# Kernel tuning notes

Hardware: AMD Instinct MI355X
Metric: run time of the kernel (lower is better)

## Reference

```python
import jax, jax.numpy as jnp
import numpy as np

B = 1024
FEAT_C = [64, 64, 128, 256, 512]    # channel dim of each intermediate feature map
SPATIAL = [1024, 1024, 256, 64, 16]  # flattened HxW of each map (32x32 input)
STRIDES = [1, 1, 2, 4, 8]
NUM_CLASS = 10


def _conv(x, w, b, s):
    y = jax.lax.conv_general_dilated(x, w, (s, s), 'SAME',
                                     dimension_numbers=('NCHW', 'OIHW', 'NCHW'))
    return y + b[None, :, None, None]


def setup_inputs() -> dict:
    key = jax.random.key(0)
    ks = iter(jax.random.split(key, 64))
    nrm = lambda shape, scale=1.0: jax.random.normal(next(ks), shape, jnp.float32) * scale
    inp = {'x': nrm((B, 3, 32, 32))}
    inp['noise_w'] = nrm((15, 3, 3, 3), 0.1)
    inp['noise_b'] = nrm((15,), 0.01)
    for i, (c, s) in enumerate(zip(FEAT_C, SPATIAL)):
        inp[f'feat_w{i}'] = nrm((c, 3, 3, 3), 0.2)
        inp[f'feat_b{i}'] = nrm((c,), 0.01)
        inp[f'mu_w{i}'] = nrm((NUM_CLASS, s), 1.0 / np.sqrt(s))
        inp[f'mu_b{i}'] = nrm((NUM_CLASS,), 0.01)
        inp[f'std_w{i}'] = nrm((NUM_CLASS, s), 1.0 / np.sqrt(s))
        inp[f'std_b{i}'] = nrm((NUM_CLASS,), 0.01)
    inp['clf_w'] = nrm((1, 5), 0.5)
    inp['clf_b'] = nrm((1,), 0.01)
    return inp


def _forward(x, noise_w, noise_b, feat_ws, feat_bs, mu_ws, mu_bs, std_ws, std_bs, clf_w, clf_b):
    Bsz = x.shape[0]
    # noised_img = x.repeat([1,5,1,1]) + noise_layer(x)   -> [B,15,32,32]
    noised = jnp.tile(x, (1, 5, 1, 1)) + _conv(x, noise_w, noise_b, 1)
    ekey = jax.random.key(42)
    scores, means, stds = [], [], []
    for i in range(5):
        xi = noised[:, 3 * i:3 * (i + 1)]
        # stand-in for pretrained_model.intermediate_forward -> [B, C_i, S_i]
        f = _conv(xi, feat_ws[i], feat_bs[i], STRIDES[i]).reshape(Bsz, FEAT_C[i], -1)
        # Linear over flattened-spatial dim then transpose(1,2): [B, 10, C_i]
        x_mean = jnp.einsum('bcs,ks->bkc', f, mu_ws[i]) + mu_bs[i][None, :, None]
        x_std = jnp.einsum('bcs,ks->bkc', f, std_ws[i]) + std_bs[i][None, :, None]
        # original builds dense diag(std)^2 [B,10,C,C]; diagonal exploited analytically
        var = x_std * x_std                       # diag entries of x_variance (== scale_tril)
        eps = jax.random.normal(jax.random.fold_in(ekey, i), x_mean.shape, x_mean.dtype)
        d = var * eps                             # sample - mean = scale_tril @ eps (diagonal)
        # -0.5 * d^T inv(diag(var)) d, inverse done analytically instead of torch.inverse
        mahal = -0.5 * jnp.sum(d * d / var, axis=-1)   # [B, 10]
        idx = jnp.argmax(mahal, axis=1)
        scores.append(jnp.max(mahal, axis=1))
        means.append(jnp.take_along_axis(x_mean, idx[:, None, None], axis=1)[:, 0, :])
        stds.append(jnp.take_along_axis(x_std, idx[:, None, None], axis=1)[:, 0, :])
    score_stack = jnp.stack(scores, axis=1)       # [B, 5]
    out = (score_stack @ clf_w.T + clf_b)[:, 0]   # classifier Linear(5,1), squeeze(-1)
    return out, means, stds


def reference(x, noise_w, noise_b,
              feat_w0, feat_b0, mu_w0, mu_b0, std_w0, std_b0,
              feat_w1, feat_b1, mu_w1, mu_b1, std_w1, std_b1,
              feat_w2, feat_b2, mu_w2, mu_b2, std_w2, std_b2,
              feat_w3, feat_b3, mu_w3, mu_b3, std_w3, std_b3,
              feat_w4, feat_b4, mu_w4, mu_b4, std_w4, std_b4,
              clf_w, clf_b):
    feat_ws = [feat_w0, feat_w1, feat_w2, feat_w3, feat_w4]
    feat_bs = [feat_b0, feat_b1, feat_b2, feat_b3, feat_b4]
    mu_ws = [mu_w0, mu_w1, mu_w2, mu_w3, mu_w4]
    mu_bs = [mu_b0, mu_b1, mu_b2, mu_b3, mu_b4]
    std_ws = [std_w0, std_w1, std_w2, std_w3, std_w4]
    std_bs = [std_b0, std_b1, std_b2, std_b3, std_b4]
    out, means, stds = _forward(x, noise_w, noise_b, feat_ws, feat_bs,
                                mu_ws, mu_bs, std_ws, std_bs, clf_w, clf_b)
    return (out, *means, *stds)
```

## Files before the change

kernel.cpp:

```cpp
#include <hip/hip_runtime.h>
#include <cstdint>

#define B_SZ 1024
#define NTHR 640

__host__ __device__ inline void tf2x32(uint32_t k0, uint32_t k1,
                                       uint32_t x0, uint32_t x1,
                                       uint32_t& o0, uint32_t& o1) {
  uint32_t ks2 = 0x1BD11BDAu ^ k0 ^ k1;
#define TF_RND(r) { x0 += x1; x1 = (x1 << (r)) | (x1 >> (32 - (r))); x1 ^= x0; }
  x0 += k0; x1 += k1;
  TF_RND(13) TF_RND(15) TF_RND(26) TF_RND(6)
  x0 += k1; x1 += ks2 + 1u;
  TF_RND(17) TF_RND(29) TF_RND(16) TF_RND(24)
  x0 += ks2; x1 += k0 + 2u;
  TF_RND(13) TF_RND(15) TF_RND(26) TF_RND(6)
  x0 += k0; x1 += k1 + 3u;
  TF_RND(17) TF_RND(29) TF_RND(16) TF_RND(24)
  x0 += k1; x1 += ks2 + 4u;
  TF_RND(13) TF_RND(15) TF_RND(26) TF_RND(6)
  x0 += ks2; x1 += k0 + 5u;
#undef TF_RND
  o0 = x0; o1 = x1;
}

__device__ inline float erfinv_f32(float x) {
  float w = -log1pf(-x * x);
  float p;
  if (w < 5.0f) {
    w -= 2.5f;
    p = 2.81022636e-08f;
    p = fmaf(p, w, 3.43273939e-07f);
    p = fmaf(p, w, -3.5233877e-06f);
    p = fmaf(p, w, -4.39150654e-06f);
    p = fmaf(p, w, 0.00021858087f);
    p = fmaf(p, w, -0.00125372503f);
    p = fmaf(p, w, -0.00417768164f);
    p = fmaf(p, w, 0.246640727f);
    p = fmaf(p, w, 1.50140941f);
  } else {
    w = sqrtf(w) - 3.0f;
    p = -0.000200214257f;
    p = fmaf(p, w, 0.000100950558f);
    p = fmaf(p, w, 0.00134934322f);
    p = fmaf(p, w, -0.00367342844f);
    p = fmaf(p, w, 0.00573950773f);
    p = fmaf(p, w, -0.0076224613f);
    p = fmaf(p, w, 0.00943887047f);
    p = fmaf(p, w, 1.00167406f);
    p = fmaf(p, w, 2.83297682f);
  }
  return p * x;
}

__device__ inline float jax_normal_pt(uint32_t k0, uint32_t k1, uint32_t e) {
  uint32_t o0, o1;
  tf2x32(k0, k1, 0u, e, o0, o1);
  uint32_t bits = o0 ^ o1;
  float f = __uint_as_float((bits >> 9) | 0x3f800000u) - 1.0f;
  const float LO = -0.99999994f;
  float u = fmaxf(LO, fmaf(f, 2.0f, LO));
  return 1.41421356f * erfinv_f32(u);
}

struct OodArgs {
  const float* x;
  const float* noise_w;
  const float* noise_b;
  const float* feat_w[5];
  const float* feat_b[5];
  const float* mu_w[5];
  const float* mu_b[5];
  const float* std_w[5];
  const float* std_b[5];
  float* mean_out[5];
  float* std_out[5];
  float* scores;
  float* gws;
  uint32_t fk0[5], fk1[5];
};

#define PITCH 35
#define CHSZ  (34 * PITCH)
#define XSZ   (3 * CHSZ)

#define A_XP   0
#define A_XI   3570
#define A_NW   7140
#define A_NB   7221
#define A_SMEM 7224

template<int S, int STRIDE>
__device__ __forceinline__ void stageA(const OodArgs& A_, float* smem, int i) {
  constexpr int Wd = 32 / STRIDE;

  const int b = blockIdx.x;
  const int t = threadIdx.x;

  float* s_xp = smem + A_XP;
  float* s_xi = smem + A_XI;
  float* s_nw = smem + A_NW;
  float* s_nb = smem + A_NB;

  for (int p = t; p < 2 * XSZ; p += NTHR) smem[p] = 0.0f;
  if (t < 81) s_nw[t] = A_.noise_w[81 * i + t];
  if (t < 3)  s_nb[t] = A_.noise_b[3 * i + t];
  __syncthreads();
  const float* xb = A_.x + (size_t)b * 3072;
  for (int p = t; p < 3072; p += NTHR) {
    int ci = p >> 10; int rr = p & 1023; int yy = rr >> 5; int xx = rr & 31;
    s_xp[ci * CHSZ + (yy + 1) * PITCH + (xx + 1)] = xb[p];
  }
  __syncthreads();

  #pragma unroll
  for (int co = 0; co < 3; ++co) {
    float nwr[27];
    #pragma unroll
    for (int j = 0; j < 27; ++j) nwr[j] = s_nw[co * 27 + j];
    const float nb = s_nb[co];
    for (int p = t; p < 1024; p += NTHR) {
      const int base = (p >> 5) * PITCH + (p & 31);
      float a = nb;
      #pragma unroll
      for (int c2 = 0; c2 < 3; ++c2) {
        #pragma unroll
        for (int q = 0; q < 9; ++q)
          a = fmaf(s_xp[c2 * CHSZ + base + (q / 3) * PITCH + (q % 3)],
                   nwr[c2 * 9 + q], a);
      }
      s_xi[co * CHSZ + base + PITCH + 1] = a + s_xp[co * CHSZ + base + PITCH + 1];
    }
  }
  __syncthreads();

  const int G  = t >> 5;
  const int ss = t & 31;
  const int wh = G & 1;
  const int kk = G >> 1;
  const float* wsrc = (wh ? A_.std_w[i] : A_.mu_w[i]) + kk * S;
  float* gdst = A_.gws + (size_t)(b * 5 + i) * 560;

  if constexpr (STRIDE == 1) {
    const float* wr = wsrc + ss * 32;
    const int rbase0 = ss * PITCH;
    #pragma unroll
    for (int ci = 0; ci < 3; ++ci) {
      const int rb = ci * CHSZ + rbase0;
      float acc[10];
      #pragma unroll
      for (int j = 0; j < 10; ++j) acc[j] = 0.0f;
      float Av[3], Bv[3], Cv[3];
      #pragma unroll
      for (int u = 0; u < 3; ++u) {
        Av[u] = s_xi[rb + u * PITCH + 0];
        Bv[u] = s_xi[rb + u * PITCH + 1];
      }

#define WCOMP(V, L) ((L) == 0 ? (V).x : (L) == 1 ? (V).y : (L) == 2 ? (V).z : (V).w)
#define STEP(X, P, Q, R, W0) { \
    _Pragma("unroll") \
    for (int u = 0; u < 3; ++u) R[u] = s_xi[rb + u * PITCH + (X) + 2]; \
    const float w0c = WCOMP(W0, (X) & 3); \
    _Pragma("unroll") \
    for (int dy = 0; dy < 3; ++dy) { \
      acc[dy*3+0] = fmaf(w0c, P[dy], acc[dy*3+0]); \
      acc[dy*3+1] = fmaf(w0c, Q[dy], acc[dy*3+1]); \
      acc[dy*3+2] = fmaf(w0c, R[dy], acc[dy*3+2]); \
    } \
    if (ci == 0) acc[9] += w0c; \
  }
#define G4_0(c) { const float4 w0 = *(const float4*)(wr + (c)); \
    STEP((c)+0, Av, Bv, Cv, w0) STEP((c)+1, Bv, Cv, Av, w0) \
    STEP((c)+2, Cv, Av, Bv, w0) STEP((c)+3, Av, Bv, Cv, w0) }
#define G4_1(c) { const float4 w0 = *(const float4*)(wr + (c)); \
    STEP((c)+0, Bv, Cv, Av, w0) STEP((c)+1, Cv, Av, Bv, w0) \
    STEP((c)+2, Av, Bv, Cv, w0) STEP((c)+3, Bv, Cv, Av, w0) }
#define G4_2(c) { const float4 w0 = *(const float4*)(wr + (c)); \
    STEP((c)+0, Cv, Av, Bv, w0) STEP((c)+1, Av, Bv, Cv, w0) \
    STEP((c)+2, Bv, Cv, Av, w0) STEP((c)+3, Cv, Av, Bv, w0) }

      G4_0(0) G4_1(4) G4_2(8) G4_0(12) G4_1(16) G4_2(20) G4_0(24) G4_1(28)

#undef G4_0
#undef G4_1
#undef G4_2
#undef STEP
#undef WCOMP
      #pragma unroll
      for (int j = 0; j < 10; ++j) {
        float v = acc[j];
        v += __shfl_xor(v,  1, 64);
        v += __shfl_xor(v,  2, 64);
        v += __shfl_xor(v,  4, 64);
        v += __shfl_xor(v,  8, 64);
        v += __shfl_xor(v, 16, 64);
        acc[j] = v;
      }
      if (ss == 0) {
        #pragma unroll
        for (int j = 0; j < 9; ++j)
          gdst[(wh * 10 + kk) * 27 + ci * 9 + j] = acc[j];
        if (ci == 0) gdst[540 + wh * 10 + kk] = acc[9];
      }
    }
  } else {
    constexpr int PER = (S >= 32) ? (S / 32) : 1;
    #pragma unroll
    for (int ci = 0; ci < 3; ++ci) {
      float acc[10];
      #pragma unroll
      for (int j = 0; j < 10; ++j) acc[j] = 0.0f;
      if (S >= 32 || ss < S) {
        #pragma unroll
        for (int u = 0; u < PER; ++u) {
          const int s  = (S >= 32) ? (ss * PER + u) : ss;
          const int yo = s / Wd, xo = s % Wd;
          const float wx = wsrc[s];
          #pragma unroll
          for (int dy = 0; dy < 3; ++dy) {
            const int base = ci * CHSZ + (yo * STRIDE + dy + 1) * PITCH + (xo * STRIDE + 1);
            #pragma unroll
            for (int dx = 0; dx < 3; ++dx)
              acc[dy * 3 + dx] = fmaf(wx, s_xi[base + dx], acc[dy * 3 + dx]);
          }
          if (ci == 0) acc[9] += wx;
        }
      }
      #pragma unroll
      for (int j = 0; j < 10; ++j) {
        float v = acc[j];
        v += __shfl_xor(v,  1, 64);
        v += __shfl_xor(v,  2, 64);
        v += __shfl_xor(v,  4, 64);
        v += __shfl_xor(v,  8, 64);
        v += __shfl_xor(v, 16, 64);
        acc[j] = v;
      }
      if (ss == 0) {
        #pragma unroll
        for (int j = 0; j < 9; ++j)
          gdst[(wh * 10 + kk) * 27 + ci * 9 + j] = acc[j];
        if (ci == 0) gdst[540 + wh * 10 + kk] = acc[9];
      }
    }
  }
}

__global__ __launch_bounds__(NTHR, 8)
void ood_a(OodArgs A_) {
  __shared__ float smem[A_SMEM];
  const int y = blockIdx.y;
  switch (y) {
    case 0:
    case 1: stageA<1024, 1>(A_, smem, y); break;
    case 2: stageA< 256, 2>(A_, smem, 2); break;
    case 3: stageA<  64, 4>(A_, smem, 3); break;
    default: stageA< 16, 8>(A_, smem, 4); break;
  }
}

template<int I, int C>
__device__ __forceinline__ void stageB(const OodArgs& A_, float* smem) {
  const int b = blockIdx.x;
  const int t = threadIdx.x;

  float* s_g   = smem;
  float* s_rs  = smem + 540;
  float* s_std = smem + 560;
  float* s_pt  = smem + 560 + 10 * C;
  int*   s_idx = (int*)(smem + 570 + 10 * C);

  const float* feat_w = A_.feat_w[I];
  const float* feat_b = A_.feat_b[I];
  const uint32_t fk0 = A_.fk0[I], fk1 = A_.fk1[I];

  const float* gsrc = A_.gws + (size_t)(b * 5 + I) * 560;
  for (int p = t; p < 560; p += 320) smem[p] = gsrc[p];
  __syncthreads();

  for (int v = t; v < 10 * C; v += 320) {
    const int k2 = v / C; const int c = v - k2 * C;
    const float* fw = feat_w + c * 27;
    float a2 = 0.0f;
    #pragma unroll
    for (int j = 0; j < 27; ++j) a2 = fmaf(s_g[(10 + k2) * 27 + j], fw[j], a2);
    a2 = fmaf(feat_b[c], s_rs[10 + k2], a2) + A_.std_b[I][k2];
    s_std[v] = a2;
  }
  __syncthreads();

  {
    const int g  = t >> 6;
    const int ln = t & 63;
    float m0 = 0.0f, m1 = 0.0f;
    for (int c = ln; c < C; c += 64) {
      {
        const float sd  = s_std[g * C + c];
        const float eps = jax_normal_pt(fk0, fk1, (uint32_t)((b * 10 + g) * C + c));
        m0 = fmaf(sd * sd, eps * eps, m0);
      }
      {
        const float sd  = s_std[(g + 5) * C + c];
        const float eps = jax_normal_pt(fk0, fk1, (uint32_t)((b * 10 + g + 5) * C + c));
        m1 = fmaf(sd * sd, eps * eps, m1);
      }
    }
    #pragma unroll
    for (int off = 32; off > 0; off >>= 1) {
      m0 += __shfl_down(m0, off, 64);
      m1 += __shfl_down(m1, off, 64);
    }
    if (ln == 0) { s_pt[g] = m0; s_pt[g + 5] = m1; }
  }
  __syncthreads();
  if (t == 0) {
    float best = -INFINITY; int bi = 0;
    #pragma unroll
    for (int k2 = 0; k2 < 10; ++k2) {
      float m = -0.5f * s_pt[k2];
      if (m > best) { best = m; bi = k2; }
    }
    A_.scores[b * 5 + I] = best;
    *s_idx = bi;
  }
  __syncthreads();

  const int idx = *s_idx;
  for (int c = t; c < C; c += 320) {
    const float* fw = feat_w + c * 27;
    float a1 = 0.0f;
    #pragma unroll
    for (int j = 0; j < 27; ++j) a1 = fmaf(s_g[idx * 27 + j], fw[j], a1);
    a1 = fmaf(feat_b[c], s_rs[idx], a1) + A_.mu_b[I][idx];
    A_.mean_out[I][(size_t)b * C + c] = a1;
    A_.std_out[I][(size_t)b * C + c]  = s_std[idx * C + c];
  }
}

__global__ __launch_bounds__(320)
void ood_b(OodArgs A_) {
  __shared__ float smem[571 + 5120];
  switch (blockIdx.y) {
    case 0: stageB<0,  64>(A_, smem); break;
    case 1: stageB<1,  64>(A_, smem); break;
    case 2: stageB<2, 128>(A_, smem); break;
    case 3: stageB<3, 256>(A_, smem); break;
    default: stageB<4, 512>(A_, smem); break;
  }
}

__global__ void ood_clf(const float* __restrict__ scores,
                        const float* __restrict__ clf_w,
                        const float* __restrict__ clf_b,
                        float* __restrict__ out) {
  int b = blockIdx.x * blockDim.x + threadIdx.x;
  if (b < B_SZ) {
    float acc = clf_b[0];
    #pragma unroll
    for (int i = 0; i < 5; ++i) acc = fmaf(scores[b * 5 + i], clf_w[i], acc);
    out[b] = acc;
  }
}

extern "C" void kernel_launch(void* const* d_in, const int* in_sizes, int n_in,
                              void* d_out, int out_size, void* d_ws, size_t ws_size,
                              hipStream_t stream) {
  (void)in_sizes; (void)n_in; (void)out_size; (void)ws_size;
  const float* clf_w = (const float*)d_in[33];
  const float* clf_b = (const float*)d_in[34];
  float* out = (float*)d_out;
  float* ws  = (float*)d_ws;

  OodArgs A_;
  A_.x       = (const float*)d_in[0];
  A_.noise_w = (const float*)d_in[1];
  A_.noise_b = (const float*)d_in[2];
  const size_t NMEAN = 1048576;
  const size_t moff[5] = {1024, 66560, 132096, 263168, 525312};
  for (int i = 0; i < 5; ++i) {
    A_.feat_w[i]   = (const float*)d_in[3 + 6 * i];
    A_.feat_b[i]   = (const float*)d_in[4 + 6 * i];
    A_.mu_w[i]     = (const float*)d_in[5 + 6 * i];
    A_.mu_b[i]     = (const float*)d_in[6 + 6 * i];
    A_.std_w[i]    = (const float*)d_in[7 + 6 * i];
    A_.std_b[i]    = (const float*)d_in[8 + 6 * i];
    A_.mean_out[i] = out + moff[i];
    A_.std_out[i]  = out + moff[i] + NMEAN;
    tf2x32(0u, 42u, 0u, (uint32_t)i, A_.fk0[i], A_.fk1[i]);
  }
  A_.scores = ws;
  A_.gws    = ws + 5120;

  ood_a<<<dim3(B_SZ, 5), NTHR, 0, stream>>>(A_);
  ood_b<<<dim3(B_SZ, 5), 320, 0, stream>>>(A_);
  ood_clf<<<(B_SZ + 255) / 256, 256, 0, stream>>>(A_.scores, clf_w, clf_b, out);
}
```

Measured before the change: 306.9 us.

## Fuse projection-collapse stage and scoring stage into one kernel via shared memory

Merges the two per-(batch, feature) kernels into a single kernel. The collapsed G and rowsum vectors stay in shared memory instead of going through a global workspace, and the std/eps/argmin stage reuses the freed image buffer region. This removes a kernel launch and the global round trip of the 560-float intermediate. The second stage now runs with 640 threads, so the eps loop handles one class per 64-lane group. The smem overlay of s_std onto the image buffers relies on the barrier placement, and the fused kernel's register and LDS needs may lower occupancy.

```diff
diff --git a/kernel.cpp b/kernel.cpp
--- a/kernel.cpp
+++ b/kernel.cpp
@@ -76,7 +76,6 @@
   float* mean_out[5];
   float* std_out[5];
   float* scores;
-  float* gws;
   uint32_t fk0[5], fk1[5];
 };
 
@@ -84,23 +83,29 @@
 #define CHSZ  (34 * PITCH)
 #define XSZ   (3 * CHSZ)
 
-#define A_XP   0
-#define A_XI   3570
-#define A_NW   7140
-#define A_NB   7221
-#define A_SMEM 7224
-
-template<int S, int STRIDE>
-__device__ __forceinline__ void stageA(const OodArgs& A_, float* smem, int i) {
+#define F_XP   0
+#define F_XI   3570
+#define F_NW   7140
+#define F_NB   7221
+#define F_G    7224
+#define F_RS   7764
+#define F_PT   7784
+#define F_IDX  7794
+#define F_SMEM 7795
+#define F_STD  0
+
+template<int S, int STRIDE, int C>
+__device__ __forceinline__ void stage_fused(const OodArgs& A_, float* smem, int i) {
   constexpr int Wd = 32 / STRIDE;
-
   const int b = blockIdx.x;
   const int t = threadIdx.x;
 
-  float* s_xp = smem + A_XP;
-  float* s_xi = smem + A_XI;
-  float* s_nw = smem + A_NW;
-  float* s_nb = smem + A_NB;
+  float* s_xp = smem + F_XP;
+  float* s_xi = smem + F_XI;
+  float* s_nw = smem + F_NW;
+  float* s_nb = smem + F_NB;
+  float* s_g  = smem + F_G;
+  float* s_rs = smem + F_RS;
 
   for (int p = t; p < 2 * XSZ; p += NTHR) smem[p] = 0.0f;
   if (t < 81) s_nw[t] = A_.noise_w[81 * i + t];
@@ -108,7 +113,7 @@
   __syncthreads();
   const float* xb = A_.x + (size_t)b * 3072;
   for (int p = t; p < 3072; p += NTHR) {
-    int ci = p >> 10; int rr = p & 1023; int yy = rr >> 5; int xx = rr & 31;
+    int ci = p >> 10, rr = p & 1023, yy = rr >> 5, xx = rr & 31;
     s_xp[ci * CHSZ + (yy + 1) * PITCH + (xx + 1)] = xb[p];
   }
   __syncthreads();
@@ -139,7 +144,29 @@
   const int wh = G & 1;
   const int kk = G >> 1;
   const float* wsrc = (wh ? A_.std_w[i] : A_.mu_w[i]) + kk * S;
-  float* gdst = A_.gws + (size_t)(b * 5 + i) * 560;
+
+#define REDUCE_WRITE(ci_) { \
+    _Pragma("unroll") \
+    for (int j = 0; j < 9; ++j) { \
+      float v = acc[j]; \
+      v += __shfl_xor(v,  1, 64); \
+      v += __shfl_xor(v,  2, 64); \
+      v += __shfl_xor(v,  4, 64); \
+      v += __shfl_xor(v,  8, 64); \
+      v += __shfl_xor(v, 16, 64); \
+      acc[j] = v; \
+    } \
+    if ((ci_) == 0) { \
+      rs += __shfl_xor(rs, 1, 64); rs += __shfl_xor(rs, 2, 64); \
+      rs += __shfl_xor(rs, 4, 64); rs += __shfl_xor(rs, 8, 64); \
+      rs += __shfl_xor(rs, 16, 64); \
+    } \
+    if (ss == 0) { \
+      _Pragma("unroll") \
+      for (int j = 0; j < 9; ++j) \
+        s_g[(wh * 10 + kk) * 27 + (ci_) * 9 + j] = acc[j]; \
+      if ((ci_) == 0) s_rs[wh * 10 + kk] = rs; \
+    } }
 
   if constexpr (STRIDE == 1) {
     const float* wr = wsrc + ss * 32;
@@ -147,9 +174,10 @@
     #pragma unroll
     for (int ci = 0; ci < 3; ++ci) {
       const int rb = ci * CHSZ + rbase0;
-      float acc[10];
+      float acc[9];
       #pragma unroll
-      for (int j = 0; j < 10; ++j) acc[j] = 0.0f;
+      for (int j = 0; j < 9; ++j) acc[j] = 0.0f;
+      float rs = 0.0f;
       float Av[3], Bv[3], Cv[3];
       #pragma unroll
       for (int u = 0; u < 3; ++u) {
@@ -168,7 +196,7 @@
       acc[dy*3+1] = fmaf(w0c, Q[dy], acc[dy*3+1]); \
       acc[dy*3+2] = fmaf(w0c, R[dy], acc[dy*3+2]); \
     } \
-    if (ci == 0) acc[9] += w0c; \
+    if (ci == 0) rs += w0c; \
   }
 #define G4_0(c) { const float4 w0 = *(const float4*)(wr + (c)); \
     STEP((c)+0, Av, Bv, Cv, w0) STEP((c)+1, Bv, Cv, Av, w0) \
@@ -187,30 +215,16 @@
 #undef G4_2
 #undef STEP
 #undef WCOMP
-      #pragma unroll
-      for (int j = 0; j < 10; ++j) {
-        float v = acc[j];
-        v += __shfl_xor(v,  1, 64);
-        v += __shfl_xor(v,  2, 64);
-        v += __shfl_xor(v,  4, 64);
-        v += __shfl_xor(v,  8, 64);
-        v += __shfl_xor(v, 16, 64);
-        acc[j] = v;
-      }
-      if (ss == 0) {
-        #pragma unroll
-        for (int j = 0; j < 9; ++j)
-          gdst[(wh * 10 + kk) * 27 + ci * 9 + j] = acc[j];
-        if (ci == 0) gdst[540 + wh * 10 + kk] = acc[9];
-      }
+      REDUCE_WRITE(ci)
     }
   } else {
     constexpr int PER = (S >= 32) ? (S / 32) : 1;
     #pragma unroll
     for (int ci = 0; ci < 3; ++ci) {
-      float acc[10];
+      float acc[9];
       #pragma unroll
-      for (int j = 0; j < 10; ++j) acc[j] = 0.0f;
+      for (int j = 0; j < 9; ++j) acc[j] = 0.0f;
+      float rs = 0.0f;
       if (S >= 32 || ss < S) {
         #pragma unroll
         for (int u = 0; u < PER; ++u) {
@@ -219,134 +233,90 @@
           const float wx = wsrc[s];
           #pragma unroll
           for (int dy = 0; dy < 3; ++dy) {
-            const int base = ci * CHSZ + (yo * STRIDE + dy + 1) * PITCH + (xo * STRIDE + 1);
+            const int ba = ci * CHSZ + (yo * STRIDE + dy + 1) * PITCH + (xo * STRIDE + 1);
             #pragma unroll
             for (int dx = 0; dx < 3; ++dx)
-              acc[dy * 3 + dx] = fmaf(wx, s_xi[base + dx], acc[dy * 3 + dx]);
+              acc[dy * 3 + dx] = fmaf(wx, s_xi[ba + dx], acc[dy * 3 + dx]);
           }
-          if (ci == 0) acc[9] += wx;
+          if (ci == 0) rs += wx;
         }
       }
-      #pragma unroll
-      for (int j = 0; j < 10; ++j) {
-        float v = acc[j];
-        v += __shfl_xor(v,  1, 64);
-        v += __shfl_xor(v,  2, 64);
-        v += __shfl_xor(v,  4, 64);
-        v += __shfl_xor(v,  8, 64);
-        v += __shfl_xor(v, 16, 64);
-        acc[j] = v;
-      }
-      if (ss == 0) {
-        #pragma unroll
-        for (int j = 0; j < 9; ++j)
-          gdst[(wh * 10 + kk) * 27 + ci * 9 + j] = acc[j];
-        if (ci == 0) gdst[540 + wh * 10 + kk] = acc[9];
-      }
-    }
+      REDUCE_WRITE(ci)
+    }
+  }
+#undef REDUCE_WRITE
+  __syncthreads();
+
+  float* s_std = smem + F_STD;
+  float* s_pt  = smem + F_PT;
+  int*   s_idx = (int*)(smem + F_IDX);
+  const float* feat_w = A_.feat_w[i];
+  const float* feat_b = A_.feat_b[i];
+
+  for (int v = t; v < 10 * C; v += NTHR) {
+    const int k2 = v / C; const int c = v & (C - 1);
+    const float* fw = feat_w + c * 27;
+    float a2 = 0.0f;
+    #pragma unroll
+    for (int j = 0; j < 27; ++j) a2 = fmaf(s_g[(10 + k2) * 27 + j], fw[j], a2);
+    a2 = fmaf(feat_b[c], s_rs[10 + k2], a2) + A_.std_b[i][k2];
+    s_std[v] = a2;
+  }
+  __syncthreads();
+
+  {
+    const int g  = t >> 6;
+    const int ln = t & 63;
+    const uint32_t fk0 = A_.fk0[i], fk1 = A_.fk1[i];
+    float m0 = 0.0f;
+    for (int c = ln; c < C; c += 64) {
+      const float sd  = s_std[g * C + c];
+      const float eps = jax_normal_pt(fk0, fk1, (uint32_t)((b * 10 + g) * C + c));
+      m0 = fmaf(sd * sd, eps * eps, m0);
+    }
+    #pragma unroll
+    for (int off = 32; off > 0; off >>= 1) m0 += __shfl_down(m0, off, 64);
+    if (ln == 0) s_pt[g] = m0;
+  }
+  __syncthreads();
+  if (t == 0) {
+    float best = -INFINITY; int bi = 0;
+    #pragma unroll
+    for (int k2 = 0; k2 < 10; ++k2) {
+      float m = -0.5f * s_pt[k2];
+      if (m > best) { best = m; bi = k2; }
+    }
+    A_.scores[b * 5 + i] = best;
+    *s_idx = bi;
+  }
+  __syncthreads();
+
+  const int idx = *s_idx;
+  float* mo = A_.mean_out[i];
+  float* so = A_.std_out[i];
+  const float mb   = A_.mu_b[i][idx];
+  const float rs0v = s_rs[idx];
+  for (int c = t; c < C; c += NTHR) {
+    const float* fw = feat_w + c * 27;
+    float a1 = 0.0f;
+    #pragma unroll
+    for (int j = 0; j < 27; ++j) a1 = fmaf(s_g[idx * 27 + j], fw[j], a1);
+    a1 = fmaf(feat_b[c], rs0v, a1) + mb;
+    mo[(size_t)b * C + c] = a1;
+    so[(size_t)b * C + c] = s_std[idx * C + c];
   }
 }
 
 __global__ __launch_bounds__(NTHR, 8)
-void ood_a(OodArgs A_) {
-  __shared__ float smem[A_SMEM];
+void ood_fused(OodArgs A_) {
+  __shared__ float smem[F_SMEM];
   const int y = blockIdx.y;
   switch (y) {
     case 0:
-    case 1: stageA<1024, 1>(A_, smem, y); break;
-    case 2: stageA< 256, 2>(A_, smem, 2); break;
-    case 3: stageA<  64, 4>(A_, smem, 3); break;
-    default: stageA< 16, 8>(A_, smem, 4); break;
-  }
-}
-
-template<int I, int C>
-__device__ __forceinline__ void stageB(const OodArgs& A_, float* smem) {
-  const int b = blockIdx.x;
-  const int t = threadIdx.x;
-
-  float* s_g   = smem;
-  float* s_rs  = smem + 540;
-  float* s_std = smem + 560;
-  float* s_pt  = smem + 560 + 10 * C;
-  int*   s_idx = (int*)(smem + 570 + 10 * C);
-
-  const float* feat_w = A_.feat_w[I];
-  const float* feat_b = A_.feat_b[I];
-  const uint32_t fk0 = A_.fk0[I], fk1 = A_.fk1[I];
-
-  const float* gsrc = A_.gws + (size_t)(b * 5 + I) * 560;
-  for (int p = t; p < 560; p += 320) smem[p] = gsrc[p];
-  __syncthreads();
-
-  for (int v = t; v < 10 * C; v += 320) {
-    const int k2 = v / C; const int c = v - k2 * C;
-    const float* fw = feat_w + c * 27;
-    float a2 = 0.0f;
-    #pragma unroll
-    for (int j = 0; j < 27; ++j) a2 = fmaf(s_g[(10 + k2) * 27 + j], fw[j], a2);
-    a2 = fmaf(feat_b[c], s_rs[10 + k2], a2) + A_.std_b[I][k2];
-    s_std[v] = a2;
-  }
-  __syncthreads();
-
-  {
-    const int g  = t >> 6;
-    const int ln = t & 63;
-    float m0 = 0.0f, m1 = 0.0f;
-    for (int c = ln; c < C; c += 64) {
-      {
-        const float sd  = s_std[g * C + c];
-        const float eps = jax_normal_pt(fk0, fk1, (uint32_t)((b * 10 + g) * C + c));
-        m0 = fmaf(sd * sd, eps * eps, m0);
-      }
-      {
-        const float sd  = s_std[(g + 5) * C + c];
-        const float eps = jax_normal_pt(fk0, fk1, (uint32_t)((b * 10 + g + 5) * C + c));
-        m1 = fmaf(sd * sd, eps * eps, m1);
-      }
-    }
-    #pragma unroll
-    for (int off = 32; off > 0; off >>= 1) {
-      m0 += __shfl_down(m0, off, 64);
-      m1 += __shfl_down(m1, off, 64);
-    }
-    if (ln == 0) { s_pt[g] = m0; s_pt[g + 5] = m1; }
-  }
-  __syncthreads();
-  if (t == 0) {
-    float best = -INFINITY; int bi = 0;
-    #pragma unroll
-    for (int k2 = 0; k2 < 10; ++k2) {
-      float m = -0.5f * s_pt[k2];
-      if (m > best) { best = m; bi = k2; }
-    }
-    A_.scores[b * 5 + I] = best;
-    *s_idx = bi;
-  }
-  __syncthreads();
-
-  const int idx = *s_idx;
-  for (int c = t; c < C; c += 320) {
-    const float* fw = feat_w + c * 27;
-    float a1 = 0.0f;
-    #pragma unroll
-    for (int j = 0; j < 27; ++j) a1 = fmaf(s_g[idx * 27 + j], fw[j], a1);
-    a1 = fmaf(feat_b[c], s_rs[idx], a1) + A_.mu_b[I][idx];
-    A_.mean_out[I][(size_t)b * C + c] = a1;
-    A_.std_out[I][(size_t)b * C + c]  = s_std[idx * C + c];
-  }
-}
-
-__global__ __launch_bounds__(320)
-void ood_b(OodArgs A_) {
-  __shared__ float smem[571 + 5120];
-  switch (blockIdx.y) {
-    case 0: stageB<0,  64>(A_, smem); break;
-    case 1: stageB<1,  64>(A_, smem); break;
-    case 2: stageB<2, 128>(A_, smem); break;
-    case 3: stageB<3, 256>(A_, smem); break;
-    default: stageB<4, 512>(A_, smem); break;
+    case 1: stage_fused<1024, 1,  64>(A_, smem, y); break;
+    case 2: stage_fused< 256, 2, 128>(A_, smem, 2); break;
+    case 3: stage_fused<  64, 4, 256>(A_, smem, 3); break;
+    default: stage_fused< 16, 8, 512>(A_, smem, 4); break;
   }
 }
 
@@ -390,9 +360,7 @@
     tf2x32(0u, 42u, 0u, (uint32_t)i, A_.fk0[i], A_.fk1[i]);
   }
   A_.scores = ws;
-  A_.gws    = ws + 5120;
-
-  ood_a<<<dim3(B_SZ, 5), NTHR, 0, stream>>>(A_);
-  ood_b<<<dim3(B_SZ, 5), 320, 0, stream>>>(A_);
+
+  ood_fused<<<dim3(B_SZ, 5), NTHR, 0, stream>>>(A_);
   ood_clf<<<(B_SZ + 255) / 256, 256, 0, stream>>>(A_.scores, clf_w, clf_b, out);
 }
```

After: 320.7 us. +4.5%, slower.

## Register-tile noise conv, vectorize smem zeroing, split stage-A kernel by stride

Applied to the files above, without the earlier changes.

The noise convolution now gives each of 384 threads an 8-pixel row segment. Each thread keeps a 10-element register window per input row and reuses it across three taps, instead of every pixel re-reading nine shared-memory values. Shared-memory zeroing uses float4 stores. Stage A is split into two kernels, one for stride-1 maps and one for strided maps, so each has less register pressure and no runtime switch. The extra launch adds a small overhead, and the strided kernel has fewer blocks.

```diff
diff --git a/kernel.cpp b/kernel.cpp
--- a/kernel.cpp
+++ b/kernel.cpp
@@ -93,7 +93,6 @@
 template<int S, int STRIDE>
 __device__ __forceinline__ void stageA(const OodArgs& A_, float* smem, int i) {
   constexpr int Wd = 32 / STRIDE;
-
   const int b = blockIdx.x;
   const int t = threadIdx.x;
 
@@ -102,35 +101,53 @@
   float* s_nw = smem + A_NW;
   float* s_nb = smem + A_NB;
 
-  for (int p = t; p < 2 * XSZ; p += NTHR) smem[p] = 0.0f;
+  {
+    float4 z; z.x = z.y = z.z = z.w = 0.0f;
+    float4* z4 = (float4*)smem;
+    for (int p = t; p < (2 * XSZ) / 4; p += NTHR) z4[p] = z;
+  }
   if (t < 81) s_nw[t] = A_.noise_w[81 * i + t];
   if (t < 3)  s_nb[t] = A_.noise_b[3 * i + t];
   __syncthreads();
   const float* xb = A_.x + (size_t)b * 3072;
   for (int p = t; p < 3072; p += NTHR) {
-    int ci = p >> 10; int rr = p & 1023; int yy = rr >> 5; int xx = rr & 31;
+    int ci = p >> 10, rr = p & 1023, yy = rr >> 5, xx = rr & 31;
     s_xp[ci * CHSZ + (yy + 1) * PITCH + (xx + 1)] = xb[p];
   }
   __syncthreads();
 
-  #pragma unroll
-  for (int co = 0; co < 3; ++co) {
-    float nwr[27];
-    #pragma unroll
-    for (int j = 0; j < 27; ++j) nwr[j] = s_nw[co * 27 + j];
+  if (t < 384) {
+    const int co = t >> 7;
+    const int r  = t & 127;
+    const int y  = r >> 2;
+    const int xs = (r & 3) * 8;
     const float nb = s_nb[co];
-    for (int p = t; p < 1024; p += NTHR) {
-      const int base = (p >> 5) * PITCH + (p & 31);
-      float a = nb;
+    float acc[8];
+    #pragma unroll
+    for (int j = 0; j < 8; ++j) acc[j] = nb;
+    #pragma unroll
+    for (int c2 = 0; c2 < 3; ++c2) {
       #pragma unroll
-      for (int c2 = 0; c2 < 3; ++c2) {
+      for (int dy = 0; dy < 3; ++dy) {
+        const float w0 = s_nw[co * 27 + c2 * 9 + dy * 3 + 0];
+        const float w1 = s_nw[co * 27 + c2 * 9 + dy * 3 + 1];
+        const float w2 = s_nw[co * 27 + c2 * 9 + dy * 3 + 2];
+        const int ra = c2 * CHSZ + (y + dy) * PITCH + xs;
+        float R[10];
         #pragma unroll
-        for (int q = 0; q < 9; ++q)
-          a = fmaf(s_xp[c2 * CHSZ + base + (q / 3) * PITCH + (q % 3)],
-                   nwr[c2 * 9 + q], a);
+        for (int u = 0; u < 10; ++u) R[u] = s_xp[ra + u];
+        #pragma unroll
+        for (int j = 0; j < 8; ++j) {
+          acc[j] = fmaf(w0, R[j],     acc[j]);
+          acc[j] = fmaf(w1, R[j + 1], acc[j]);
+          acc[j] = fmaf(w2, R[j + 2], acc[j]);
+        }
       }
-      s_xi[co * CHSZ + base + PITCH + 1] = a + s_xp[co * CHSZ + base + PITCH + 1];
-    }
+    }
+    const int ob = co * CHSZ + (y + 1) * PITCH + (xs + 1);
+    #pragma unroll
+    for (int j = 0; j < 8; ++j)
+      s_xi[ob + j] = acc[j] + s_xp[ob + j];
   }
   __syncthreads();
 
@@ -141,15 +158,39 @@
   const float* wsrc = (wh ? A_.std_w[i] : A_.mu_w[i]) + kk * S;
   float* gdst = A_.gws + (size_t)(b * 5 + i) * 560;
 
+#define REDUCE_WRITE(ci_) { \
+    _Pragma("unroll") \
+    for (int j = 0; j < 9; ++j) { \
+      float v = acc[j]; \
+      v += __shfl_xor(v,  1, 64); \
+      v += __shfl_xor(v,  2, 64); \
+      v += __shfl_xor(v,  4, 64); \
+      v += __shfl_xor(v,  8, 64); \
+      v += __shfl_xor(v, 16, 64); \
+      acc[j] = v; \
+    } \
+    if ((ci_) == 0) { \
+      rs += __shfl_xor(rs, 1, 64); rs += __shfl_xor(rs, 2, 64); \
+      rs += __shfl_xor(rs, 4, 64); rs += __shfl_xor(rs, 8, 64); \
+      rs += __shfl_xor(rs, 16, 64); \
+    } \
+    if (ss == 0) { \
+      _Pragma("unroll") \
+      for (int j = 0; j < 9; ++j) \
+        gdst[(wh * 10 + kk) * 27 + (ci_) * 9 + j] = acc[j]; \
+      if ((ci_) == 0) gdst[540 + wh * 10 + kk] = rs; \
+    } }
+
   if constexpr (STRIDE == 1) {
     const float* wr = wsrc + ss * 32;
     const int rbase0 = ss * PITCH;
     #pragma unroll
     for (int ci = 0; ci < 3; ++ci) {
       const int rb = ci * CHSZ + rbase0;
-      float acc[10];
+      float acc[9];
       #pragma unroll
-      for (int j = 0; j < 10; ++j) acc[j] = 0.0f;
+      for (int j = 0; j < 9; ++j) acc[j] = 0.0f;
+      float rs = 0.0f;
       float Av[3], Bv[3], Cv[3];
       #pragma unroll
       for (int u = 0; u < 3; ++u) {
@@ -168,7 +209,7 @@
       acc[dy*3+1] = fmaf(w0c, Q[dy], acc[dy*3+1]); \
       acc[dy*3+2] = fmaf(w0c, R[dy], acc[dy*3+2]); \
     } \
-    if (ci == 0) acc[9] += w0c; \
+    if (ci == 0) rs += w0c; \
   }
 #define G4_0(c) { const float4 w0 = *(const float4*)(wr + (c)); \
     STEP((c)+0, Av, Bv, Cv, w0) STEP((c)+1, Bv, Cv, Av, w0) \
@@ -187,30 +228,16 @@
 #undef G4_2
 #undef STEP
 #undef WCOMP
-      #pragma unroll
-      for (int j = 0; j < 10; ++j) {
-        float v = acc[j];
-        v += __shfl_xor(v,  1, 64);
-        v += __shfl_xor(v,  2, 64);
-        v += __shfl_xor(v,  4, 64);
-        v += __shfl_xor(v,  8, 64);
-        v += __shfl_xor(v, 16, 64);
-        acc[j] = v;
-      }
-      if (ss == 0) {
-        #pragma unroll
-        for (int j = 0; j < 9; ++j)
-          gdst[(wh * 10 + kk) * 27 + ci * 9 + j] = acc[j];
-        if (ci == 0) gdst[540 + wh * 10 + kk] = acc[9];
-      }
+      REDUCE_WRITE(ci)
     }
   } else {
     constexpr int PER = (S >= 32) ? (S / 32) : 1;
     #pragma unroll
     for (int ci = 0; ci < 3; ++ci) {
-      float acc[10];
+      float acc[9];
       #pragma unroll
-      for (int j = 0; j < 10; ++j) acc[j] = 0.0f;
+      for (int j = 0; j < 9; ++j) acc[j] = 0.0f;
+      float rs = 0.0f;
       if (S >= 32 || ss < S) {
         #pragma unroll
         for (int u = 0; u < PER; ++u) {
@@ -219,43 +246,32 @@
           const float wx = wsrc[s];
           #pragma unroll
           for (int dy = 0; dy < 3; ++dy) {
-            const int base = ci * CHSZ + (yo * STRIDE + dy + 1) * PITCH + (xo * STRIDE + 1);
+            const int ba = ci * CHSZ + (yo * STRIDE + dy + 1) * PITCH + (xo * STRIDE + 1);
             #pragma unroll
             for (int dx = 0; dx < 3; ++dx)
-              acc[dy * 3 + dx] = fmaf(wx, s_xi[base + dx], acc[dy * 3 + dx]);
+              acc[dy * 3 + dx] = fmaf(wx, s_xi[ba + dx], acc[dy * 3 + dx]);
           }
-          if (ci == 0) acc[9] += wx;
+          if (ci == 0) rs += wx;
         }
       }
-      #pragma unroll
-      for (int j = 0; j < 10; ++j) {
-        float v = acc[j];
-        v += __shfl_xor(v,  1, 64);
-        v += __shfl_xor(v,  2, 64);
-        v += __shfl_xor(v,  4, 64);
-        v += __shfl_xor(v,  8, 64);
-        v += __shfl_xor(v, 16, 64);
-        acc[j] = v;
-      }
-      if (ss == 0) {
-        #pragma unroll
-        for (int j = 0; j < 9; ++j)
-          gdst[(wh * 10 + kk) * 27 + ci * 9 + j] = acc[j];
-        if (ci == 0) gdst[540 + wh * 10 + kk] = acc[9];
-      }
-    }
-  }
+      REDUCE_WRITE(ci)
+    }
+  }
+#undef REDUCE_WRITE
 }
 
 __global__ __launch_bounds__(NTHR, 8)
-void ood_a(OodArgs A_) {
-  __shared__ float smem[A_SMEM];
-  const int y = blockIdx.y;
-  switch (y) {
-    case 0:
-    case 1: stageA<1024, 1>(A_, smem, y); break;
-    case 2: stageA< 256, 2>(A_, smem, 2); break;
-    case 3: stageA<  64, 4>(A_, smem, 3); break;
+void ood_a_s1(OodArgs A_) {
+  __shared__ __align__(16) float smem[A_SMEM];
+  stageA<1024, 1>(A_, smem, blockIdx.y);
+}
+
+__global__ __launch_bounds__(NTHR, 8)
+void ood_a_sN(OodArgs A_) {
+  __shared__ __align__(16) float smem[A_SMEM];
+  switch (blockIdx.y) {
+    case 0:  stageA<256, 2>(A_, smem, 2); break;
+    case 1:  stageA< 64, 4>(A_, smem, 3); break;
     default: stageA< 16, 8>(A_, smem, 4); break;
   }
 }
@@ -392,7 +408,8 @@
   A_.scores = ws;
   A_.gws    = ws + 5120;
 
-  ood_a<<<dim3(B_SZ, 5), NTHR, 0, stream>>>(A_);
+  ood_a_s1<<<dim3(B_SZ, 2), NTHR, 0, stream>>>(A_);
+  ood_a_sN<<<dim3(B_SZ, 3), NTHR, 0, stream>>>(A_);
   ood_b<<<dim3(B_SZ, 5), 320, 0, stream>>>(A_);
   ood_clf<<<(B_SZ + 255) / 256, 256, 0, stream>>>(A_.scores, clf_w, clf_b, out);
 }
```

After: 317.8 us. 3.6% more time.
